# Optimization experiments

Hardware: AMD Instinct MI355X
Metric: run time of the kernel (lower is better)

## Reference

```python
import jax, jax.numpy as jnp
import numpy as np
from jax import lax

V_TH = 1.0    # base firing threshold
RHO = 0.9     # adaptive-threshold decay
ADAPT = 0.1   # threshold increment per spike
SLOPE = 5.0   # surrogate-gradient sigmoid slope

@jax.custom_vjp
def spike_fn(v):
    return (v >= 0.0).astype(v.dtype)

def _spike_fwd(v):
    return spike_fn(v), v

def _spike_bwd(v, g):
    s = jax.nn.sigmoid(SLOPE * v)
    return (g * SLOPE * s * (1.0 - s),)

spike_fn.defvjp(_spike_fwd, _spike_bwd)

def lif_scan(x_seq, beta):
    # x_seq: (T, ..., F) channel-last; beta: (F,). Adaptive LIF with soft reset.
    def step(carry, x):
        mem, b = carry
        mem = beta * mem + x
        th = V_TH + b
        spk = spike_fn(mem - th)
        mem = mem - spk * th
        b = RHO * b + ADAPT * spk
        return (mem, b), spk
    z = jnp.zeros_like(x_seq[0])
    _, spikes = lax.scan(step, (z, z), x_seq)
    return spikes

def conv2d_s2(x, w, b):
    # NCHW conv, stride 2, padding 1
    y = lax.conv_general_dilated(x, w, (2, 2), ((1, 1), (1, 1)),
                                 dimension_numbers=('NCHW', 'OIHW', 'NCHW'))
    return y + b[None, :, None, None]

def mha(x, wq, wk, wv, wo, nh=4):
    B, T, D = x.shape
    dh = D // nh
    q = (x @ wq.T).reshape(B, T, nh, dh)
    k = (x @ wk.T).reshape(B, T, nh, dh)
    v = (x @ wv.T).reshape(B, T, nh, dh)
    att = jnp.einsum('bqhd,bkhd->bhqk', q, k) * (dh ** -0.5)
    p = jax.nn.softmax(att, axis=-1)
    o = jnp.einsum('bhqk,bkhd->bqhd', p, v).reshape(B, T, D)
    return o @ wo.T

def _forward(x, conv1_w, conv1_b, conv2_w, conv2_b, beta1, beta2,
             proj_w, proj_b, wq, wk, wv, wo, cls_w, cls_b):
    B, T, C, H, W = x.shape
    H1, W1, H2, W2 = H // 2, W // 2, H // 4, W // 4
    # stage 1 conv over all timesteps at once (conv is stateless)
    c1 = conv2d_s2(x.reshape(B * T, C, H, W), conv1_w, conv1_b)       # (B*T,16,H1,W1)
    c1 = jnp.moveaxis(c1.reshape(B, T, 16, H1, W1), 2, -1)            # (B,T,H1,W1,16)
    c1 = jnp.moveaxis(c1, 1, 0)                                       # (T,B,H1,W1,16)
    s1 = lif_scan(c1, beta1)                                          # (T,B,H1,W1,16)
    s1 = jnp.moveaxis(jnp.moveaxis(s1, 0, 1), -1, 2)                  # (B,T,16,H1,W1)
    # stage 2
    c2 = conv2d_s2(s1.reshape(B * T, 16, H1, W1), conv2_w, conv2_b)   # (B*T,32,H2,W2)
    c2 = jnp.moveaxis(c2.reshape(B, T, 32, H2, W2), 2, -1)
    c2 = jnp.moveaxis(c2, 1, 0)                                       # (T,B,H2,W2,32)
    s2 = lif_scan(c2, beta2)                                          # (T,B,H2,W2,32)
    total_spikes = s2.sum()
    # flatten channel-major to match torch permute(0,3,1,2).view(B,-1)
    feats = jnp.moveaxis(s2, -1, 2)                                   # (T,B,32,H2,W2)
    feats = jnp.moveaxis(feats, 0, 1).reshape(B, T, -1)               # (B,T,32*H2*W2)
    proj = feats @ proj_w.T + proj_b                                  # (B,T,64)
    attn = mha(proj, wq, wk, wv, wo)                                  # (B,T,64)
    context = attn.mean(axis=1)                                       # (B,64)
    # lif_out single step from zero state: mem = context
    spk_out = spike_fn(context - V_TH)
    logits = spk_out @ cls_w.T + cls_b
    sparsity = 1.0 - total_spikes / float(feats.size)
    return logits, sparsity

def setup_inputs() -> dict:
    key = jax.random.key(0)
    ks = jax.random.split(key, 10)
    B, T, C, H, W = 64, 8, 2, 128, 128
    D = 64
    flat = 32 * (H // 4) * (W // 4)  # 32768
    f = jnp.float32
    return {
        'x': (jax.random.uniform(ks[0], (B, T, C, H, W)) < 0.1).astype(f),  # sparse DVS events
        'conv1_w': jax.random.normal(ks[1], (16, C, 3, 3), f) * 0.2,
        'conv1_b': jnp.zeros((16,), f),
        'conv2_w': jax.random.normal(ks[2], (32, 16, 3, 3), f) * 0.1,
        'conv2_b': jnp.zeros((32,), f),
        'beta1': jnp.full((16,), 0.9, f),
        'beta2': jnp.full((32,), 0.9, f),
        'proj_w': jax.random.normal(ks[3], (D, flat), f) * (flat ** -0.5),
        'proj_b': jnp.zeros((D,), f),
        'wq': jax.random.normal(ks[4], (D, D), f) * (D ** -0.5),
        'wk': jax.random.normal(ks[5], (D, D), f) * (D ** -0.5),
        'wv': jax.random.normal(ks[6], (D, D), f) * (D ** -0.5),
        'wo': jax.random.normal(ks[7], (D, D), f) * (D ** -0.5),
        'cls_w': jax.random.normal(ks[8], (2, D), f) * (D ** -0.5),
        'cls_b': jnp.zeros((2,), f),
    }

def reference(x, conv1_w, conv1_b, conv2_w, conv2_b, beta1, beta2,
              proj_w, proj_b, wq, wk, wv, wo, cls_w, cls_b):
    return _forward(x, conv1_w, conv1_b, conv2_w, conv2_b, beta1, beta2,
                    proj_w, proj_b, wq, wk, wv, wo, cls_w, cls_b)
```

## Files before the change

### kernel.cpp

```cpp
#include <hip/hip_runtime.h>
#include <cstdint>

#define V_TH 1.0f
#define RHO 0.9f
#define ADAPT 0.1f

static constexpr int B = 64, T = 8, C = 2, H = 128, W = 128;
static constexpr int H1 = 64, W1 = 64;
static constexpr int H2 = 32, W2 = 32;
static constexpr int FLAT = 32 * H2 * W2;
static constexpr int R = B * T;

static constexpr size_t OFF_TRIP  = 0;
static constexpr size_t OFF_BITS  = OFF_TRIP + 8388608;
static constexpr size_t OFF_PWT   = OFF_BITS + 2097152;
static constexpr size_t OFF_CNT   = OFF_PWT + 8388608;
static constexpr size_t OFF_TBL   = OFF_CNT + 256;
static constexpr size_t OFF_PART  = OFF_TBL + 6291456;

__global__ __launch_bounds__(256) void k_mega1(
    const float* __restrict__ x, const float* __restrict__ w,
    const float* __restrict__ bias, const float* __restrict__ beta,
    uint64_t* __restrict__ trip,
    const float* __restrict__ pw, float* __restrict__ pwt,
    const float* __restrict__ c2w, float* __restrict__ tbl,
    unsigned int* __restrict__ cnt) {
  __shared__ __align__(16) float shmem[64 * 65];
  int bid = blockIdx.x;
  int tid = threadIdx.x;
  if (bid < 1024) {
    float4* tb = (float4*)shmem;
    float* sww = shmem + 3072;
    for (int i = tid; i < 288; i += 256) sww[i] = w[i];
    __syncthreads();
    if (tid < 192) {
      int kh = tid >> 6, v = tid & 63;
      float e[16];
#pragma unroll
      for (int c = 0; c < 16; ++c) e[c] = 0.f;
#pragma unroll
      for (int bbit = 0; bbit < 6; ++bbit) {
        if ((v >> bbit) & 1) {
          int ci = (bbit >= 3) ? 1 : 0;
          int kw = bbit - ci * 3;
          int base = ci * 9 + kh * 3 + kw;
#pragma unroll
          for (int c = 0; c < 16; ++c) e[c] += sww[c * 18 + base];
        }
      }
#pragma unroll
      for (int s = 0; s < 4; ++s)
        tb[(kh * 4 + s) * 64 + v] =
            make_float4(e[4 * s], e[4 * s + 1], e[4 * s + 2], e[4 * s + 3]);
    }
    __syncthreads();

    int gid = bid * 256 + tid;
    int w1 = gid & 63, h1 = (gid >> 6) & 63, b = gid >> 12;
    int lane = tid & 63;
    (void)w1;
    float bias_r[16], beta_r[16];
#pragma unroll
    for (int c = 0; c < 16; ++c) { bias_r[c] = bias[c]; beta_r[c] = beta[c]; }
    float mem[16], bth[16];
#pragma unroll
    for (int c = 0; c < 16; ++c) { mem[c] = 0.f; bth[c] = 0.f; }

    int y0 = 2 * h1 - 1;
    bool vtop = (y0 >= 0);
    const float* xb = x + (size_t)(b * T) * 2 * 16384 + 2 * lane;

    float2 cur[6];
#pragma unroll
    for (int ci = 0; ci < 2; ++ci)
#pragma unroll
      for (int kh = 0; kh < 3; ++kh) {
        int j = ci * 3 + kh;
        cur[j] = (kh == 0 && !vtop) ? make_float2(0.f, 0.f)
               : *(const float2*)(xb + ci * 16384 + (y0 + kh) * 128);
      }

    for (int t = 0; t < T; ++t) {
      int r = b * T + t;
      float2 nxt[6];
      if (t + 1 < T) {
        const float* xn = xb + (size_t)(t + 1) * 32768;
#pragma unroll
        for (int ci = 0; ci < 2; ++ci)
#pragma unroll
          for (int kh = 0; kh < 3; ++kh) {
            int j = ci * 3 + kh;
            nxt[j] = (kh == 0 && !vtop) ? make_float2(0.f, 0.f)
                   : *(const float2*)(xn + ci * 16384 + (y0 + kh) * 128);
          }
      }
      uint32_t Mc = 0, Rr = 0;
#pragma unroll
      for (int j = 0; j < 6; ++j) {
        uint32_t bm = (cur[j].x != 0.f) ? 1u : 0u;
        uint32_t br = (cur[j].y != 0.f) ? 1u : 0u;
        Mc |= ((bm << 1) | (br << 2)) << (3 * j);
        Rr |= br << j;
      }
      uint32_t RL = (uint32_t)__shfl((int)Rr, lane - 1, 64);
      if (lane == 0) RL = 0u;
      uint32_t M = Mc | (RL & 1u) | ((RL & 2u) << 2) | ((RL & 4u) << 4)
                 | ((RL & 8u) << 6) | ((RL & 16u) << 8) | ((RL & 32u) << 10);
      int i0 = (int)((M & 7u)         | (((M >> 9) & 7u) << 3));
      int i1 = (int)(((M >> 3) & 7u)  | (((M >> 12) & 7u) << 3));
      int i2 = (int)(((M >> 6) & 7u)  | (((M >> 15) & 7u) << 3));
      float acc[16];
#pragma unroll
      for (int s = 0; s < 4; ++s) {
        float4 u0 = tb[s * 64 + i0];
        float4 u1 = tb[(4 + s) * 64 + i1];
        float4 u2 = tb[(8 + s) * 64 + i2];
        acc[4 * s + 0] = bias_r[4 * s + 0] + u0.x + u1.x + u2.x;
        acc[4 * s + 1] = bias_r[4 * s + 1] + u0.y + u1.y + u2.y;
        acc[4 * s + 2] = bias_r[4 * s + 2] + u0.z + u1.z + u2.z;
        acc[4 * s + 3] = bias_r[4 * s + 3] + u0.w + u1.w + u2.w;
      }
      uint32_t mask = 0;
#pragma unroll
      for (int c = 0; c < 16; ++c) {
        mem[c] = beta_r[c] * mem[c] + acc[c];
        float th = V_TH + bth[c];
        bool s = (mem[c] >= th);
        if (s) { mem[c] -= th; mask |= (1u << c); }
        bth[c] = RHO * bth[c] + (s ? ADAPT : 0.f);
      }
      int iL = 2 * lane - 1; if (iL < 0) iL = 0;
      uint32_t mL = __shfl((int)mask, iL, 64);
      uint32_t mC = __shfl((int)mask, 2 * lane, 64);
      uint32_t mR = __shfl((int)mask, 2 * lane + 1, 64);
      if (lane < 32) {
        uint64_t tw = (uint64_t)(lane ? mL : 0u) | ((uint64_t)mC << 16) |
                      ((uint64_t)mR << 32);
        trip[(size_t)(r * H1 + h1) * 32 + lane] = tw;
      }
      if (t + 1 < T) {
#pragma unroll
        for (int j = 0; j < 6; ++j) cur[j] = nxt[j];
      }
    }
  } else if (bid < 1536) {
    float* tile = shmem;
    int tb = bid - 1024;
    int c = tb >> 4, pt = tb & 15;
    int posc = ((c & 3) << 3) + (c >> 2);
    int p0 = pt * 64;
    int lane = tid & 63, quad = tid >> 6;
#pragma unroll
    for (int it = 0; it < 16; ++it) {
      int d = it * 4 + quad;
      tile[d * 65 + lane] = pw[(size_t)d * FLAT + c * 1024 + p0 + lane];
    }
    __syncthreads();
#pragma unroll
    for (int it = 0; it < 16; ++it) {
      int pp = it * 4 + quad;
      pwt[((size_t)((p0 + pp) * 32 + posc)) * 64 + lane] = tile[lane * 65 + pp];
    }
  } else if (bid == 1536) {
    if (tid == 0) *cnt = 0u;
  } else {
    int idx = bid - 1537;
    int g = idx >> 4;
    int kh = g >> 2, gp = g & 3;
    int v = ((idx & 15) << 8) + tid;
    float e[32];
#pragma unroll
    for (int co = 0; co < 32; ++co) e[co] = 0.f;
    for (int i = 0; i < 12; ++i) {
      if ((v >> i) & 1) {
        int j = gp * 12 + i;
        int kw = j >> 4, ci = j & 15;
#pragma unroll
        for (int co = 0; co < 32; ++co)
          e[co] += c2w[((co * 16 + ci) * 3 + kh) * 3 + kw];
      }
    }
#pragma unroll
    for (int co = 0; co < 32; ++co)
      tbl[((size_t)(g * 4096 + v)) * 32 + co] = e[co];
  }
}

__global__ __launch_bounds__(256) void k_conv2_lif2(
    const uint64_t* __restrict__ trip, const float* __restrict__ tbl,
    const float* __restrict__ bias, const float* __restrict__ beta,
    uint32_t* __restrict__ bits, unsigned int* __restrict__ cnt) {
  __shared__ unsigned int sc;
  int tid = threadIdx.x;
  if (tid == 0) sc = 0u;
  __syncthreads();
  int lane = tid & 63;
  int li = lane & 7;
  int p8 = lane >> 3;
  int wvi = (blockIdx.x * 256 + tid) >> 6;
  int px = wvi * 8 + p8;
  int w2 = px & 31, h2 = (px >> 5) & 31, b = px >> 10;
  float4 b4 = *(const float4*)&bias[4 * li];
  float4 bt4 = *(const float4*)&beta[4 * li];
  float m0v = 0.f, m1v = 0.f, m2v = 0.f, m3v = 0.f;
  float t0 = 0.f, t1 = 0.f, t2 = 0.f, t3 = 0.f;
  unsigned int lc = 0;
  const float4* tb4 = (const float4*)tbl;
  for (int t = 0; t < T; ++t) {
    int r = b * T + t;
    const uint64_t* tr = trip + (size_t)(r * 64 + 2 * h2) * 32 + w2;
    uint64_t q0 = (h2 > 0) ? tr[-32] : 0ull;
    uint64_t q1 = tr[0];
    uint64_t q2 = tr[32];
    uint32_t r0l = (uint32_t)q0, r0h = (uint32_t)(q0 >> 32);
    uint32_t r1l = (uint32_t)q1, r1h = (uint32_t)(q1 >> 32);
    uint32_t r2l = (uint32_t)q2, r2h = (uint32_t)(q2 >> 32);
    float4 v0 = tb4[(0 << 15) + ((r0l & 4095u) << 3) + li];
    float4 v1 = tb4[(1 << 15) + (((r0l >> 12) & 4095u) << 3) + li];
    float4 v2 = tb4[(2 << 15) + ((((r0l >> 24) | (r0h << 8)) & 4095u) << 3) + li];
    float4 v3 = tb4[(3 << 15) + (((r0h >> 4) & 4095u) << 3) + li];
    float4 v4 = tb4[(4 << 15) + ((r1l & 4095u) << 3) + li];
    float4 v5 = tb4[(5 << 15) + (((r1l >> 12) & 4095u) << 3) + li];
    float4 v6 = tb4[(6 << 15) + ((((r1l >> 24) | (r1h << 8)) & 4095u) << 3) + li];
    float4 v7 = tb4[(7 << 15) + (((r1h >> 4) & 4095u) << 3) + li];
    float4 v8 = tb4[(8 << 15) + ((r2l & 4095u) << 3) + li];
    float4 v9 = tb4[(9 << 15) + (((r2l >> 12) & 4095u) << 3) + li];
    float4 va = tb4[(10 << 15) + ((((r2l >> 24) | (r2h << 8)) & 4095u) << 3) + li];
    float4 vb = tb4[(11 << 15) + (((r2h >> 4) & 4095u) << 3) + li];
    float A0 = b4.x + v0.x + v1.x + v2.x + v3.x;
    float A1 = b4.y + v0.y + v1.y + v2.y + v3.y;
    float A2 = b4.z + v0.z + v1.z + v2.z + v3.z;
    float A3 = b4.w + v0.w + v1.w + v2.w + v3.w;
    float B0 = v4.x + v5.x + v6.x + v7.x;
    float B1 = v4.y + v5.y + v6.y + v7.y;
    float B2 = v4.z + v5.z + v6.z + v7.z;
    float B3 = v4.w + v5.w + v6.w + v7.w;
    float C0 = v8.x + v9.x + va.x + vb.x;
    float C1 = v8.y + v9.y + va.y + vb.y;
    float C2 = v8.z + v9.z + va.z + vb.z;
    float C3 = v8.w + v9.w + va.w + vb.w;
    float a0 = (A0 + B0) + C0, a1 = (A1 + B1) + C1;
    float a2 = (A2 + B2) + C2, a3 = (A3 + B3) + C3;
    m0v = bt4.x * m0v + a0;
    m1v = bt4.y * m1v + a1;
    m2v = bt4.z * m2v + a2;
    m3v = bt4.w * m3v + a3;
    float th0 = V_TH + t0, th1 = V_TH + t1, th2 = V_TH + t2, th3 = V_TH + t3;
    bool s0 = (m0v >= th0), s1 = (m1v >= th1), s2 = (m2v >= th2), s3 = (m3v >= th3);
    if (s0) m0v -= th0;
    if (s1) m1v -= th1;
    if (s2) m2v -= th2;
    if (s3) m3v -= th3;
    t0 = RHO * t0 + (s0 ? ADAPT : 0.f);
    t1 = RHO * t1 + (s1 ? ADAPT : 0.f);
    t2 = RHO * t2 + (s2 ? ADAPT : 0.f);
    t3 = RHO * t3 + (s3 ? ADAPT : 0.f);
    unsigned long long bl0 = __ballot(s0);
    unsigned long long bl1 = __ballot(s1);
    unsigned long long bl2 = __ballot(s2);
    unsigned long long bl3 = __ballot(s3);
    if (li == 0) {
      int sh = p8 * 8;
      uint32_t m32 = ((uint32_t)(bl0 >> sh) & 0xFFu)
                   | (((uint32_t)(bl1 >> sh) & 0xFFu) << 8)
                   | (((uint32_t)(bl2 >> sh) & 0xFFu) << 16)
                   | (((uint32_t)(bl3 >> sh) & 0xFFu) << 24);
      bits[(size_t)r * 1024 + (px & 1023)] = m32;
      lc += __popc(m32);
    }
  }
  if (li == 0) atomicAdd(&sc, lc);
  __syncthreads();
  if (tid == 0) atomicAdd(cnt, sc);
}

__global__ __launch_bounds__(256) void k_proj_gemm(
    const uint32_t* __restrict__ bits, const float* __restrict__ pwt,
    float* __restrict__ partial) {
  int rt = blockIdx.x >> 4;
  int ks = (blockIdx.x & 15) * 4 + (threadIdx.x >> 6);
  int d = threadIdx.x & 63;
  float acc[8] = {0, 0, 0, 0, 0, 0, 0, 0};
  const uint32_t* bb = bits + (size_t)rt * 8 * 1024;
  for (int wi = 0; wi < 16; ++wi) {
    int word = ks * 16 + wi;
    const float* rowbase = pwt + ((size_t)word * 32) * 64 + d;
#pragma unroll
    for (int ri = 0; ri < 8; ++ri) {
      uint32_t m = bb[ri * 1024 + word];
      while (m) {
        int c = __ffs(m) - 1; m &= m - 1;
        acc[ri] += rowbase[c << 6];
      }
    }
  }
#pragma unroll
  for (int ri = 0; ri < 8; ++ri)
    partial[((size_t)(rt * 64 + ks) * 8 + ri) * 64 + d] = acc[ri];
}

__global__ __launch_bounds__(256) void k_attn_final(
    const float* __restrict__ partial, const float* __restrict__ pb,
    const float* __restrict__ wq, const float* __restrict__ wk,
    const float* __restrict__ wv, const float* __restrict__ wo,
    const float* __restrict__ clsw, const float* __restrict__ clsb,
    const unsigned int* __restrict__ cnt, float* __restrict__ out) {
  __shared__ float swq[64 * 65], swk[64 * 65], swv[64 * 65], swo[64 * 65];
  __shared__ float sp[8 * 65], sq[8 * 65], sk[8 * 65], sv[8 * 65], so2[8 * 65];
  __shared__ float satt[4][8][8];
  __shared__ float sob[64];
  int b = blockIdx.x, tid = threadIdx.x;
  for (int i = tid; i < 4096; i += 256) {
    int dd = i >> 6, e = i & 63;
    swq[dd * 65 + e] = wq[i]; swk[dd * 65 + e] = wk[i];
    swv[dd * 65 + e] = wv[i]; swo[dd * 65 + e] = wo[i];
  }
  for (int i = tid; i < 512; i += 256) {
    int ri = i >> 6, d = i & 63;
    float s = pb[d];
    const float* p = partial + ((size_t)(b * 64) * 8 + ri) * 64 + d;
#pragma unroll
    for (int ks = 0; ks < 64; ++ks) s += p[(size_t)ks * 512];
    sp[ri * 65 + d] = s;
  }
  __syncthreads();
#pragma unroll
  for (int p = 0; p < 2; ++p) {
    int idx = p * 256 + tid, t = idx >> 6, d = idx & 63;
    float qa = 0.f, ka = 0.f, va = 0.f;
    for (int e = 0; e < 64; ++e) {
      float pe = sp[t * 65 + e];
      qa += pe * swq[d * 65 + e];
      ka += pe * swk[d * 65 + e];
      va += pe * swv[d * 65 + e];
    }
    sq[t * 65 + d] = qa; sk[t * 65 + d] = ka; sv[t * 65 + d] = va;
  }
  __syncthreads();
  {
    int h = tid >> 6, q = (tid >> 3) & 7, k = tid & 7;
    float s = 0.f;
    for (int j = 0; j < 16; ++j)
      s += sq[q * 65 + h * 16 + j] * sk[k * 65 + h * 16 + j];
    satt[h][q][k] = s * 0.25f;
  }
  __syncthreads();
  if (tid < 32) {
    int h = tid >> 3, q2 = tid & 7;
    float m = -1e30f;
    for (int k2 = 0; k2 < 8; ++k2) m = fmaxf(m, satt[h][q2][k2]);
    float sum = 0.f;
    for (int k2 = 0; k2 < 8; ++k2) {
      float e = expf(satt[h][q2][k2] - m);
      satt[h][q2][k2] = e; sum += e;
    }
    float inv = 1.f / sum;
    for (int k2 = 0; k2 < 8; ++k2) satt[h][q2][k2] *= inv;
  }
  __syncthreads();
#pragma unroll
  for (int p = 0; p < 2; ++p) {
    int idx = p * 256 + tid, t = idx >> 6, d = idx & 63;
    int h = d >> 4;
    float o = 0.f;
    for (int k = 0; k < 8; ++k) o += satt[h][t][k] * sv[k * 65 + d];
    so2[t * 65 + d] = o;
  }
  __syncthreads();
  if (tid < 64) {
    float ob = 0.f;
    for (int t = 0; t < 8; ++t) ob += so2[t * 65 + tid];
    sob[tid] = ob * 0.125f;
  }
  __syncthreads();
  if (tid < 64) {
    float ctx = 0.f;
    for (int e = 0; e < 64; ++e) ctx += sob[e] * swo[tid * 65 + e];
    int spk = (ctx >= V_TH) ? 1 : 0;
    unsigned long long ball = __ballot(spk);
    if (tid < 2) {
      float lg = clsb[tid];
      for (int dd = 0; dd < 64; ++dd)
        if ((ball >> dd) & 1ull) lg += clsw[tid * 64 + dd];
      out[b * 2 + tid] = lg;
    }
    if (b == 0 && tid == 2)
      out[128] = 1.f - (float)(*cnt) / 16777216.f;
  }
}

extern "C" void kernel_launch(void* const* d_in, const int* in_sizes, int n_in,
                              void* d_out, int out_size, void* d_ws, size_t ws_size,
                              hipStream_t stream) {
  const float* x    = (const float*)d_in[0];
  const float* c1w  = (const float*)d_in[1];
  const float* c1b  = (const float*)d_in[2];
  const float* c2w  = (const float*)d_in[3];
  const float* c2b  = (const float*)d_in[4];
  const float* bt1  = (const float*)d_in[5];
  const float* bt2  = (const float*)d_in[6];
  const float* pw   = (const float*)d_in[7];
  const float* pb   = (const float*)d_in[8];
  const float* wq   = (const float*)d_in[9];
  const float* wk   = (const float*)d_in[10];
  const float* wv   = (const float*)d_in[11];
  const float* wo   = (const float*)d_in[12];
  const float* clsw = (const float*)d_in[13];
  const float* clsb = (const float*)d_in[14];
  float* out = (float*)d_out;

  uint8_t* ws = (uint8_t*)d_ws;
  uint64_t* trip  = (uint64_t*)(ws + OFF_TRIP);
  uint32_t* bits  = (uint32_t*)(ws + OFF_BITS);
  float*    pwt   = (float*)(ws + OFF_PWT);
  unsigned int* cnt = (unsigned int*)(ws + OFF_CNT);
  float*    tbl   = (float*)(ws + OFF_TBL);
  float*    part  = (float*)(ws + OFF_PART);

  k_mega1<<<1729, 256, 0, stream>>>(x, c1w, c1b, bt1, trip, pw, pwt, c2w, tbl, cnt);
  k_conv2_lif2<<<2048, 256, 0, stream>>>(trip, tbl, c2b, bt2, bits, cnt);
  k_proj_gemm<<<1024, 256, 0, stream>>>(bits, pwt, part);
  k_attn_final<<<64, 256, 0, stream>>>(part, pb, wq, wk, wv, wo, clsw, clsb, cnt, out);
}
```

Baseline: 206.2 us.

## Split conv1+LIF1 channels across two waves per row to double parallelism

The stage-1 conv+LIF work is now split so two wavefronts handle each output row, each owning 8 of the 16 channels. The two halves exchange spike masks through shared memory with a per-timestep block barrier before the triplet words are packed and written. The bias is folded into the lookup table, the next-timestep prefetch is dropped, and launch bounds request more resident blocks. The goal is to halve per-thread register state and double the block count to improve occupancy and latency hiding, at the cost of duplicated input loads and a __syncthreads inside the time loop.

```diff
diff --git a/kernel.cpp b/kernel.cpp
--- a/kernel.cpp
+++ b/kernel.cpp
@@ -18,7 +18,7 @@
 static constexpr size_t OFF_TBL   = OFF_CNT + 256;
 static constexpr size_t OFF_PART  = OFF_TBL + 6291456;
 
-__global__ __launch_bounds__(256) void k_mega1(
+__global__ __launch_bounds__(256, 6) void k_mega1(
     const float* __restrict__ x, const float* __restrict__ w,
     const float* __restrict__ bias, const float* __restrict__ beta,
     uint64_t* __restrict__ trip,
@@ -28,9 +28,10 @@
   __shared__ __align__(16) float shmem[64 * 65];
   int bid = blockIdx.x;
   int tid = threadIdx.x;
-  if (bid < 1024) {
-    float4* tb = (float4*)shmem;
-    float* sww = shmem + 3072;
+  if (bid < 2048) {
+    float2* t2 = (float2*)shmem;
+    uint32_t* smask = (uint32_t*)(shmem + 3072);
+    float* sww = shmem + 3328;
     for (int i = tid; i < 288; i += 256) sww[i] = w[i];
     __syncthreads();
     if (tid < 192) {
@@ -48,60 +49,54 @@
           for (int c = 0; c < 16; ++c) e[c] += sww[c * 18 + base];
         }
       }
-#pragma unroll
-      for (int s = 0; s < 4; ++s)
-        tb[(kh * 4 + s) * 64 + v] =
-            make_float4(e[4 * s], e[4 * s + 1], e[4 * s + 2], e[4 * s + 3]);
+      if (kh == 0) {
+#pragma unroll
+        for (int c = 0; c < 16; ++c) e[c] += bias[c];
+      }
+#pragma unroll
+      for (int p = 0; p < 8; ++p)
+        t2[(kh * 8 + p) * 64 + v] = make_float2(e[2 * p], e[2 * p + 1]);
     }
     __syncthreads();
 
-    int gid = bid * 256 + tid;
-    int w1 = gid & 63, h1 = (gid >> 6) & 63, b = gid >> 12;
-    int lane = tid & 63;
-    (void)w1;
-    float bias_r[16], beta_r[16];
-#pragma unroll
-    for (int c = 0; c < 16; ++c) { bias_r[c] = bias[c]; beta_r[c] = beta[c]; }
-    float mem[16], bth[16];
-#pragma unroll
-    for (int c = 0; c < 16; ++c) { mem[c] = 0.f; bth[c] = 0.f; }
+    int wv = tid >> 6, lane = tid & 63;
+    int hc = wv & 1, rowi = wv >> 1;
+    int row_lin = bid * 2 + rowi;
+    int h1 = row_lin & 63, b = row_lin >> 6;
+    int hb = hc * 4;
+
+    float beta_r[8];
+    {
+      float4 q0 = *(const float4*)&beta[hc * 8];
+      float4 q1 = *(const float4*)&beta[hc * 8 + 4];
+      beta_r[0] = q0.x; beta_r[1] = q0.y; beta_r[2] = q0.z; beta_r[3] = q0.w;
+      beta_r[4] = q1.x; beta_r[5] = q1.y; beta_r[6] = q1.z; beta_r[7] = q1.w;
+    }
+    float mem[8], bth[8];
+#pragma unroll
+    for (int c = 0; c < 8; ++c) { mem[c] = 0.f; bth[c] = 0.f; }
 
     int y0 = 2 * h1 - 1;
     bool vtop = (y0 >= 0);
     const float* xb = x + (size_t)(b * T) * 2 * 16384 + 2 * lane;
 
-    float2 cur[6];
-#pragma unroll
-    for (int ci = 0; ci < 2; ++ci)
-#pragma unroll
-      for (int kh = 0; kh < 3; ++kh) {
-        int j = ci * 3 + kh;
-        cur[j] = (kh == 0 && !vtop) ? make_float2(0.f, 0.f)
-               : *(const float2*)(xb + ci * 16384 + (y0 + kh) * 128);
-      }
-
     for (int t = 0; t < T; ++t) {
       int r = b * T + t;
-      float2 nxt[6];
-      if (t + 1 < T) {
-        const float* xn = xb + (size_t)(t + 1) * 32768;
-#pragma unroll
-        for (int ci = 0; ci < 2; ++ci)
-#pragma unroll
-          for (int kh = 0; kh < 3; ++kh) {
-            int j = ci * 3 + kh;
-            nxt[j] = (kh == 0 && !vtop) ? make_float2(0.f, 0.f)
-                   : *(const float2*)(xn + ci * 16384 + (y0 + kh) * 128);
-          }
-      }
+      const float* xt = xb + (size_t)t * 32768;
       uint32_t Mc = 0, Rr = 0;
 #pragma unroll
-      for (int j = 0; j < 6; ++j) {
-        uint32_t bm = (cur[j].x != 0.f) ? 1u : 0u;
-        uint32_t br = (cur[j].y != 0.f) ? 1u : 0u;
-        Mc |= ((bm << 1) | (br << 2)) << (3 * j);
-        Rr |= br << j;
-      }
+      for (int ci = 0; ci < 2; ++ci)
+#pragma unroll
+        for (int kh = 0; kh < 3; ++kh) {
+          int j = ci * 3 + kh;
+          float2 v = (kh == 0 && !vtop)
+                         ? make_float2(0.f, 0.f)
+                         : *(const float2*)(xt + ci * 16384 + (y0 + kh) * 128);
+          uint32_t bm = (v.x != 0.f) ? 1u : 0u;
+          uint32_t br = (v.y != 0.f) ? 1u : 0u;
+          Mc |= ((bm << 1) | (br << 2)) << (3 * j);
+          Rr |= br << j;
+        }
       uint32_t RL = (uint32_t)__shfl((int)Rr, lane - 1, 64);
       if (lane == 0) RL = 0u;
       uint32_t M = Mc | (RL & 1u) | ((RL & 2u) << 2) | ((RL & 4u) << 4)
@@ -109,43 +104,51 @@
       int i0 = (int)((M & 7u)         | (((M >> 9) & 7u) << 3));
       int i1 = (int)(((M >> 3) & 7u)  | (((M >> 12) & 7u) << 3));
       int i2 = (int)(((M >> 6) & 7u)  | (((M >> 15) & 7u) << 3));
-      float acc[16];
-#pragma unroll
-      for (int s = 0; s < 4; ++s) {
-        float4 u0 = tb[s * 64 + i0];
-        float4 u1 = tb[(4 + s) * 64 + i1];
-        float4 u2 = tb[(8 + s) * 64 + i2];
-        acc[4 * s + 0] = bias_r[4 * s + 0] + u0.x + u1.x + u2.x;
-        acc[4 * s + 1] = bias_r[4 * s + 1] + u0.y + u1.y + u2.y;
-        acc[4 * s + 2] = bias_r[4 * s + 2] + u0.z + u1.z + u2.z;
-        acc[4 * s + 3] = bias_r[4 * s + 3] + u0.w + u1.w + u2.w;
-      }
+      float2 a0 = t2[(hb + 0) * 64 + i0];
+      float2 a1 = t2[(hb + 1) * 64 + i0];
+      float2 a2 = t2[(hb + 2) * 64 + i0];
+      float2 a3 = t2[(hb + 3) * 64 + i0];
+      float2 b0 = t2[512 + (hb + 0) * 64 + i1];
+      float2 b1 = t2[512 + (hb + 1) * 64 + i1];
+      float2 b2 = t2[512 + (hb + 2) * 64 + i1];
+      float2 b3 = t2[512 + (hb + 3) * 64 + i1];
+      float2 c0 = t2[1024 + (hb + 0) * 64 + i2];
+      float2 c1 = t2[1024 + (hb + 1) * 64 + i2];
+      float2 c2 = t2[1024 + (hb + 2) * 64 + i2];
+      float2 c3 = t2[1024 + (hb + 3) * 64 + i2];
+      float acc[8];
+      acc[0] = (a0.x + b0.x) + c0.x;  acc[1] = (a0.y + b0.y) + c0.y;
+      acc[2] = (a1.x + b1.x) + c1.x;  acc[3] = (a1.y + b1.y) + c1.y;
+      acc[4] = (a2.x + b2.x) + c2.x;  acc[5] = (a2.y + b2.y) + c2.y;
+      acc[6] = (a3.x + b3.x) + c3.x;  acc[7] = (a3.y + b3.y) + c3.y;
       uint32_t mask = 0;
 #pragma unroll
-      for (int c = 0; c < 16; ++c) {
+      for (int c = 0; c < 8; ++c) {
         mem[c] = beta_r[c] * mem[c] + acc[c];
         float th = V_TH + bth[c];
         bool s = (mem[c] >= th);
         if (s) { mem[c] -= th; mask |= (1u << c); }
         bth[c] = RHO * bth[c] + (s ? ADAPT : 0.f);
       }
-      int iL = 2 * lane - 1; if (iL < 0) iL = 0;
-      uint32_t mL = __shfl((int)mask, iL, 64);
-      uint32_t mC = __shfl((int)mask, 2 * lane, 64);
-      uint32_t mR = __shfl((int)mask, 2 * lane + 1, 64);
-      if (lane < 32) {
-        uint64_t tw = (uint64_t)(lane ? mL : 0u) | ((uint64_t)mC << 16) |
-                      ((uint64_t)mR << 32);
-        trip[(size_t)(r * H1 + h1) * 32 + lane] = tw;
-      }
-      if (t + 1 < T) {
-#pragma unroll
-        for (int j = 0; j < 6; ++j) cur[j] = nxt[j];
-      }
-    }
-  } else if (bid < 1536) {
+      int sIdx = ((t & 1) << 7) + (rowi << 6) + lane;
+      if (hc == 1) smask[sIdx] = mask;
+      __syncthreads();
+      if (hc == 0) {
+        uint32_t full = mask | (smask[sIdx] << 8);
+        int iL = 2 * lane - 1; if (iL < 0) iL = 0;
+        uint32_t mL = __shfl((int)full, iL, 64);
+        uint32_t mC = __shfl((int)full, 2 * lane, 64);
+        uint32_t mR = __shfl((int)full, 2 * lane + 1, 64);
+        if (lane < 32) {
+          uint64_t tw = (uint64_t)(lane ? mL : 0u) | ((uint64_t)mC << 16) |
+                        ((uint64_t)mR << 32);
+          trip[(size_t)(r * H1 + h1) * 32 + lane] = tw;
+        }
+      }
+    }
+  } else if (bid < 2560) {
     float* tile = shmem;
-    int tb = bid - 1024;
+    int tb = bid - 2048;
     int c = tb >> 4, pt = tb & 15;
     int posc = ((c & 3) << 3) + (c >> 2);
     int p0 = pt * 64;
@@ -161,10 +164,10 @@
       int pp = it * 4 + quad;
       pwt[((size_t)((p0 + pp) * 32 + posc)) * 64 + lane] = tile[lane * 65 + pp];
     }
-  } else if (bid == 1536) {
+  } else if (bid == 2560) {
     if (tid == 0) *cnt = 0u;
   } else {
-    int idx = bid - 1537;
+    int idx = bid - 2561;
     int g = idx >> 4;
     int kh = g >> 2, gp = g & 3;
     int v = ((idx & 15) << 8) + tid;
@@ -417,7 +420,7 @@
   float*    tbl   = (float*)(ws + OFF_TBL);
   float*    part  = (float*)(ws + OFF_PART);
 
-  k_mega1<<<1729, 256, 0, stream>>>(x, c1w, c1b, bt1, trip, pw, pwt, c2w, tbl, cnt);
+  k_mega1<<<2753, 256, 0, stream>>>(x, c1w, c1b, bt1, trip, pw, pwt, c2w, tbl, cnt);
   k_conv2_lif2<<<2048, 256, 0, stream>>>(trip, tbl, c2b, bt2, bits, cnt);
   k_proj_gemm<<<1024, 256, 0, stream>>>(bits, pwt, part);
   k_attn_final<<<64, 256, 0, stream>>>(part, pb, wq, wk, wv, wo, clsw, clsb, cnt, out);
```

Result: slower. 221.0 us (+7.1%).

## Deepen input prefetch to two steps, fold bias into LUT, pad LUT layout

Applied to the files above, without the earlier changes.

In the first stage of the mega kernel, the per-timestep input loads now prefetch two timesteps ahead using a 3-slot register ring, and the time loop is fully unrolled. The bias is folded into the kh=0 lookup-table entries, which removes the per-step bias adds and the bias registers. The LUT is restructured as per-index rows of 9 float2 (stride padded) to reduce LDS bank conflicts on data-dependent gathers. A launch-bounds occupancy hint of 4 is added, which may trade registers for occupancy and could cause spills.

```diff
diff --git a/kernel.cpp b/kernel.cpp
--- a/kernel.cpp
+++ b/kernel.cpp
@@ -18,7 +18,7 @@
 static constexpr size_t OFF_TBL   = OFF_CNT + 256;
 static constexpr size_t OFF_PART  = OFF_TBL + 6291456;
 
-__global__ __launch_bounds__(256) void k_mega1(
+__global__ __launch_bounds__(256, 4) void k_mega1(
     const float* __restrict__ x, const float* __restrict__ w,
     const float* __restrict__ bias, const float* __restrict__ beta,
     uint64_t* __restrict__ trip,
@@ -29,8 +29,8 @@
   int bid = blockIdx.x;
   int tid = threadIdx.x;
   if (bid < 1024) {
-    float4* tb = (float4*)shmem;
-    float* sww = shmem + 3072;
+    float2* t2 = (float2*)shmem;
+    float* sww = shmem + 3456;
     for (int i = tid; i < 288; i += 256) sww[i] = w[i];
     __syncthreads();
     if (tid < 192) {
@@ -48,20 +48,22 @@
           for (int c = 0; c < 16; ++c) e[c] += sww[c * 18 + base];
         }
       }
-#pragma unroll
-      for (int s = 0; s < 4; ++s)
-        tb[(kh * 4 + s) * 64 + v] =
-            make_float4(e[4 * s], e[4 * s + 1], e[4 * s + 2], e[4 * s + 3]);
+      if (kh == 0) {
+#pragma unroll
+        for (int c = 0; c < 16; ++c) e[c] += bias[c];
+      }
+#pragma unroll
+      for (int p = 0; p < 8; ++p)
+        t2[(kh * 64 + v) * 9 + p] = make_float2(e[2 * p], e[2 * p + 1]);
     }
     __syncthreads();
 
     int gid = bid * 256 + tid;
-    int w1 = gid & 63, h1 = (gid >> 6) & 63, b = gid >> 12;
+    int h1 = (gid >> 6) & 63, b = gid >> 12;
     int lane = tid & 63;
-    (void)w1;
-    float bias_r[16], beta_r[16];
-#pragma unroll
-    for (int c = 0; c < 16; ++c) { bias_r[c] = bias[c]; beta_r[c] = beta[c]; }
+    float beta_r[16];
+#pragma unroll
+    for (int c = 0; c < 16; ++c) beta_r[c] = beta[c];
     float mem[16], bth[16];
 #pragma unroll
     for (int c = 0; c < 16; ++c) { mem[c] = 0.f; bth[c] = 0.f; }
@@ -70,35 +72,43 @@
     bool vtop = (y0 >= 0);
     const float* xb = x + (size_t)(b * T) * 2 * 16384 + 2 * lane;
 
-    float2 cur[6];
-#pragma unroll
-    for (int ci = 0; ci < 2; ++ci)
-#pragma unroll
-      for (int kh = 0; kh < 3; ++kh) {
-        int j = ci * 3 + kh;
-        cur[j] = (kh == 0 && !vtop) ? make_float2(0.f, 0.f)
-               : *(const float2*)(xb + ci * 16384 + (y0 + kh) * 128);
-      }
-
+    float2 buf[3][6];
+#pragma unroll
+    for (int tt = 0; tt < 2; ++tt) {
+      const float* xn = xb + (size_t)tt * 32768;
+#pragma unroll
+      for (int ci = 0; ci < 2; ++ci)
+#pragma unroll
+        for (int kh = 0; kh < 3; ++kh) {
+          int j = ci * 3 + kh;
+          buf[tt][j] = (kh == 0 && !vtop)
+                           ? make_float2(0.f, 0.f)
+                           : *(const float2*)(xn + ci * 16384 + (y0 + kh) * 128);
+        }
+    }
+
+#pragma unroll
     for (int t = 0; t < T; ++t) {
+      const int cs = t % 3, ns = (t + 2) % 3;
       int r = b * T + t;
-      float2 nxt[6];
-      if (t + 1 < T) {
-        const float* xn = xb + (size_t)(t + 1) * 32768;
+      if (t + 2 < T) {
+        const float* xn = xb + (size_t)(t + 2) * 32768;
 #pragma unroll
         for (int ci = 0; ci < 2; ++ci)
 #pragma unroll
           for (int kh = 0; kh < 3; ++kh) {
             int j = ci * 3 + kh;
-            nxt[j] = (kh == 0 && !vtop) ? make_float2(0.f, 0.f)
-                   : *(const float2*)(xn + ci * 16384 + (y0 + kh) * 128);
+            buf[ns][j] = (kh == 0 && !vtop)
+                             ? make_float2(0.f, 0.f)
+                             : *(const float2*)(xn + ci * 16384 + (y0 + kh) * 128);
           }
       }
       uint32_t Mc = 0, Rr = 0;
 #pragma unroll
       for (int j = 0; j < 6; ++j) {
-        uint32_t bm = (cur[j].x != 0.f) ? 1u : 0u;
-        uint32_t br = (cur[j].y != 0.f) ? 1u : 0u;
+        float2 v = buf[cs][j];
+        uint32_t bm = (v.x != 0.f) ? 1u : 0u;
+        uint32_t br = (v.y != 0.f) ? 1u : 0u;
         Mc |= ((bm << 1) | (br << 2)) << (3 * j);
         Rr |= br << j;
       }
@@ -109,16 +119,21 @@
       int i0 = (int)((M & 7u)         | (((M >> 9) & 7u) << 3));
       int i1 = (int)(((M >> 3) & 7u)  | (((M >> 12) & 7u) << 3));
       int i2 = (int)(((M >> 6) & 7u)  | (((M >> 15) & 7u) << 3));
+      const float2* T0p = t2 + (size_t)i0 * 9;
+      const float2* T1p = t2 + (size_t)(64 + i1) * 9;
+      const float2* T2p = t2 + (size_t)(128 + i2) * 9;
+      float2 Av[8], Bv[8], Cv[8];
+#pragma unroll
+      for (int p = 0; p < 8; ++p) Av[p] = T0p[p];
+#pragma unroll
+      for (int p = 0; p < 8; ++p) Bv[p] = T1p[p];
+#pragma unroll
+      for (int p = 0; p < 8; ++p) Cv[p] = T2p[p];
       float acc[16];
 #pragma unroll
-      for (int s = 0; s < 4; ++s) {
-        float4 u0 = tb[s * 64 + i0];
-        float4 u1 = tb[(4 + s) * 64 + i1];
-        float4 u2 = tb[(8 + s) * 64 + i2];
-        acc[4 * s + 0] = bias_r[4 * s + 0] + u0.x + u1.x + u2.x;
-        acc[4 * s + 1] = bias_r[4 * s + 1] + u0.y + u1.y + u2.y;
-        acc[4 * s + 2] = bias_r[4 * s + 2] + u0.z + u1.z + u2.z;
-        acc[4 * s + 3] = bias_r[4 * s + 3] + u0.w + u1.w + u2.w;
+      for (int p = 0; p < 8; ++p) {
+        acc[2 * p]     = (Av[p].x + Bv[p].x) + Cv[p].x;
+        acc[2 * p + 1] = (Av[p].y + Bv[p].y) + Cv[p].y;
       }
       uint32_t mask = 0;
 #pragma unroll
@@ -137,10 +152,6 @@
         uint64_t tw = (uint64_t)(lane ? mL : 0u) | ((uint64_t)mC << 16) |
                       ((uint64_t)mR << 32);
         trip[(size_t)(r * H1 + h1) * 32 + lane] = tw;
-      }
-      if (t + 1 < T) {
-#pragma unroll
-        for (int j = 0; j < 6; ++j) cur[j] = nxt[j];
       }
     }
   } else if (bid < 1536) {
```

Measured after the change: 215.7 us. +4.6%, slower.
